# Kernel optimization log

Hardware: AMD Instinct MI355X
Metric: run time of the kernel (lower is better)

## Reference

```python
import jax, jax.numpy as jnp
import numpy as np

B, L, D, H, F = 2, 1024, 1024, 16, 4096
DH = D // H
EPS = 1e-6


def _layernorm(x, g, b, eps=1e-5):
    m = jnp.mean(x, axis=-1, keepdims=True)
    v = jnp.mean((x - m) ** 2, axis=-1, keepdims=True)
    return (x - m) / jnp.sqrt(v + eps) * g + b


def setup_inputs() -> dict:
    key = jax.random.key(0)
    ks = jax.random.split(key, 12)

    def w(k, shape):
        return jax.random.normal(k, shape, dtype=jnp.float32) * 0.02

    return {
        "inputs": jax.random.normal(ks[0], (B, L, D), dtype=jnp.float32),
        "attn_mask": jnp.zeros((L, L), dtype=jnp.bool_),
        "Wq": w(ks[1], (D, D)), "bq": jnp.zeros((D,), jnp.float32),
        "Wk": w(ks[2], (D, D)), "bk": jnp.zeros((D,), jnp.float32),
        "Wv": w(ks[3], (D, D)), "bv": jnp.zeros((D,), jnp.float32),
        "Wo": w(ks[4], (D, D)), "bo": jnp.zeros((D,), jnp.float32),
        "ln1_g": jnp.ones((D,), jnp.float32), "ln1_b": jnp.zeros((D,), jnp.float32),
        "W1": w(ks[5], (D, F)), "b1": jnp.zeros((F,), jnp.float32),
        "W2": w(ks[6], (F, D)), "b2": jnp.zeros((D,), jnp.float32),
        "ln2_g": jnp.ones((D,), jnp.float32), "ln2_b": jnp.zeros((D,), jnp.float32),
    }


def _decoder_layer(inputs, Wq, bq, Wk, bk, Wv, bv, Wo, bo,
                   ln1_g, ln1_b, W1, b1, W2, b2, ln2_g, ln2_b):
    Bn, Ln, Dn = inputs.shape

    def heads(W, b):
        # [B,L,D] -> [B,H,L,Dh]
        return (inputs @ W + b).reshape(Bn, Ln, H, DH).transpose(0, 2, 1, 3)

    q = jax.nn.sigmoid(heads(Wq, bq))  # kernel feature map
    k = jax.nn.sigmoid(heads(Wk, bk))
    v = heads(Wv, bv)

    normal = (jnp.arange(Ln, dtype=jnp.float32) + 1.0)[None, None, :]  # [1,1,L]

    sink_in = normal / jnp.einsum('bhld,bhld->bhl', q + EPS, jnp.cumsum(k, axis=2) + EPS)
    src_out = normal / jnp.einsum('bhld,bhld->bhl', k + EPS, jnp.cumsum(q, axis=2) + EPS)

    cons_sink = jnp.einsum('bhld,bhld->bhl', q + EPS,
                           jnp.cumsum(k * src_out[..., None], axis=2) + EPS) / normal
    cons_src = jnp.einsum('bhld,bhld->bhl', k + EPS,
                          jnp.cumsum(q * sink_in[..., None], axis=2) + EPS) / normal
    cons_src = jnp.clip(cons_src, -1.0, 1.0)

    sink_alloc = jax.nn.sigmoid(cons_sink)
    cons_src = jnp.exp(cons_src)
    src_comp = cons_src / jnp.cumsum(cons_src, axis=-1) * normal

    # causal linear attention: cumsum of outer products k v^T, contracted with q
    qs = q * (sink_in / normal)[..., None]           # [B,H,L,Dh]
    vs = v * src_comp[..., None]                     # [B,H,L,Dh]
    kv = jnp.cumsum(jnp.einsum('bhld,bhlm->bhldm', k, vs), axis=2)  # [B,H,L,Dh,Dh]
    x = jnp.einsum('bhld,bhldm->bhlm', qs, kv) * sink_alloc[..., None]

    x = x.transpose(0, 2, 1, 3).reshape(Bn, Ln, Dn)
    attn = x @ Wo + bo

    h = _layernorm(inputs + attn, ln1_g, ln1_b)
    ffn = jax.nn.gelu(h @ W1 + b1, approximate=False) @ W2 + b2
    return _layernorm(h + ffn, ln2_g, ln2_b)


def reference(inputs, attn_mask, Wq, bq, Wk, bk, Wv, bv, Wo, bo,
              ln1_g, ln1_b, W1, b1, W2, b2, ln2_g, ln2_b):
    # attn_mask is unused by the original module (causality comes from cumsum)
    return _decoder_layer(inputs, Wq, bq, Wk, bk, Wv, bv, Wo, bo,
                          ln1_g, ln1_b, W1, b1, W2, b2, ln2_g, ln2_b)
```

## Files before the change

### kernel.cpp

```cpp
#include <hip/hip_runtime.h>
#include <hip/hip_bf16.h>

#define EPS 1e-6f
#define NBH 32
#define LSEQ 1024
#define DHD 64

typedef unsigned short u16;
typedef __bf16 bf16x8 __attribute__((ext_vector_type(8)));
typedef float f32x4 __attribute__((ext_vector_type(4)));

__device__ inline u16 f2bf(float f){
  union { float f; unsigned u; } un; un.f = f;
  unsigned u = un.u;
  u += 0x7fffu + ((u >> 16) & 1u);
  return (u16)(u >> 16);
}

__device__ inline float wred64(float v){
#pragma unroll
  for (int off = 32; off > 0; off >>= 1) v += __shfl_xor(v, off, 64);
  return v;
}

__device__ inline float wscan64(float v, int lane){
  float run = v;
#pragma unroll
  for (int off = 1; off < 64; off <<= 1){
    float t = __shfl_up(run, off, 64);
    if (lane >= off) run += t;
  }
  return run;
}

__device__ inline float fast_sigmoid(float x){
  return 1.f / (1.f + __expf(-x));
}

__device__ inline void gload_lds16(const u16* g, u16* l){
  __builtin_amdgcn_global_load_lds(
      (const __attribute__((address_space(1))) unsigned int*)g,
      (__attribute__((address_space(3))) unsigned int*)l, 16, 0, 0);
}

__global__ __launch_bounds__(256) void f2bf_kernel(const float* __restrict__ in,
                                                   u16* __restrict__ out, int n4){
  int i = blockIdx.x * 256 + threadIdx.x;
  if (i < n4){
    float4 v = reinterpret_cast<const float4*>(in)[i];
    ushort4 o; o.x = f2bf(v.x); o.y = f2bf(v.y); o.z = f2bf(v.z); o.w = f2bf(v.w);
    reinterpret_cast<ushort4*>(out)[i] = o;
  }
}

__device__ inline void tr_tile2(const float* in, u16* out, int R, int C, int r0, int c0){
  __shared__ float tile[32][33];
  int x = threadIdx.x & 31, y = threadIdx.x >> 5;
#pragma unroll
  for (int j = 0; j < 4; j++)
    tile[y + j*8][x] = in[(size_t)(r0 + y + j*8) * C + c0 + x];
  __syncthreads();
#pragma unroll
  for (int j = 0; j < 4; j++)
    out[(size_t)(c0 + y + j*8) * R + r0 + x] = f2bf(tile[x][y + j*8]);
}

__global__ __launch_bounds__(256) void transpose4_f2bf(
    const float* __restrict__ w0, const float* __restrict__ w1,
    const float* __restrict__ w2, const float* __restrict__ w3,
    u16* __restrict__ dqkv, u16* __restrict__ dwo){
  int z = blockIdx.z;
  const float* in = (z == 0) ? w0 : (z == 1) ? w1 : (z == 2) ? w2 : w3;
  u16* out = (z < 3) ? (dqkv + (size_t)z * 1024 * 1024) : dwo;
  tr_tile2(in, out, 1024, 1024, blockIdx.y * 32, blockIdx.x * 32);
}

__global__ __launch_bounds__(256) void transpose2_f2bf(
    const float* __restrict__ w1, const float* __restrict__ w2,
    u16* __restrict__ d1, u16* __restrict__ d2){
  if (blockIdx.z == 0)
    tr_tile2(w1, d1, 1024, 4096, blockIdx.y * 32, blockIdx.x * 32);
  else
    tr_tile2(w2, d2, 4096, 1024, blockIdx.x * 32, blockIdx.y * 32);
}

__global__ __launch_bounds__(256) void bias_gather(const float* __restrict__ bq,
                                                   const float* __restrict__ bk,
                                                   const float* __restrict__ bv,
                                                   float* __restrict__ dst){
  int i = blockIdx.x * 256 + threadIdx.x;
  if (i < 3072){
    float v = (i < 1024) ? bq[i] : (i < 2048) ? bk[i - 1024] : bv[i - 2048];
    dst[i] = v;
  }
}

template<int BM, int BN, int ACT, int OM>
__global__ __launch_bounds__(256) void gemm_mfma(
    const u16* __restrict__ A, const u16* __restrict__ Bt,
    const float* __restrict__ bias, const float* __restrict__ resid,
    float* __restrict__ outF, u16* __restrict__ outB,
    int M, int N, int K)
{
  constexpr int BK = 64;
  constexpr int MI = BM / 32;
  constexpr int NJ = BN / 32;
  constexpr int RA = BM / 32;
  constexpr int RB = BN / 32;
  __shared__ u16 As[BM * BK];
  __shared__ u16 Bs[BN * BK];
  const int tid = threadIdx.x;
  const int lane = tid & 63, wave = tid >> 6;
  const int lrow = lane & 15, lg = lane >> 4;
  const int m0 = blockIdx.x * BM, n0 = blockIdx.y * BN;
  const int wm = (wave >> 1) * (BM / 2), wn = (wave & 1) * (BN / 2);

  const int ksz = K / gridDim.z;
  const int k_begin = blockIdx.z * ksz;
  const int k_end = k_begin + ksz;

  f32x4 acc[MI][NJ];
#pragma unroll
  for (int i = 0; i < MI; i++)
#pragma unroll
    for (int j = 0; j < NJ; j++) acc[i][j] = (f32x4){0.f, 0.f, 0.f, 0.f};

  const u16* Ab = A + (size_t)m0 * K;
  const u16* Bb = Bt + (size_t)n0 * K;

  const int s0 = ((0 * 4 + lg) ^ (lrow & 7)) * 8;
  const int s1 = ((1 * 4 + lg) ^ (lrow & 7)) * 8;

  for (int k0 = k_begin; k0 < k_end; k0 += BK){
    __syncthreads();
#pragma unroll
    for (int r = 0; r < RA; ++r){
      int c = r * 256 + tid;
      int row = c >> 3;
      int kk = ((c ^ row) & 7) << 3;
      gload_lds16(Ab + (size_t)row * K + k0 + kk, &As[(r * 256 + wave * 64) * 8]);
    }
#pragma unroll
    for (int r = 0; r < RB; ++r){
      int c = r * 256 + tid;
      int row = c >> 3;
      int kk = ((c ^ row) & 7) << 3;
      gload_lds16(Bb + (size_t)row * K + k0 + kk, &Bs[(r * 256 + wave * 64) * 8]);
    }
    __syncthreads();
#pragma unroll
    for (int kh = 0; kh < 2; ++kh){
      const int ss = (kh == 0) ? s0 : s1;
      bf16x8 af[MI], bfv[NJ];
#pragma unroll
      for (int i = 0; i < MI; ++i)
        af[i] = *reinterpret_cast<const bf16x8*>(&As[(wm + i * 16 + lrow) * BK + ss]);
#pragma unroll
      for (int j = 0; j < NJ; ++j)
        bfv[j] = *reinterpret_cast<const bf16x8*>(&Bs[(wn + j * 16 + lrow) * BK + ss]);
#pragma unroll
      for (int i = 0; i < MI; ++i)
#pragma unroll
        for (int j = 0; j < NJ; ++j)
          acc[i][j] = __builtin_amdgcn_mfma_f32_16x16x32_bf16(af[i], bfv[j], acc[i][j], 0, 0, 0);
    }
  }

#pragma unroll
  for (int i = 0; i < MI; ++i){
#pragma unroll
    for (int j = 0; j < NJ; ++j){
      int col = n0 + wn + j * 16 + lrow;
      float bv = (OM != 4 && bias) ? bias[col] : 0.f;
#pragma unroll
      for (int r = 0; r < 4; ++r){
        int row = m0 + wm + i * 16 + lg * 4 + r;
        float x = acc[i][j][r] + bv;
        if (OM == 1){
          if (col < 2048) x = fast_sigmoid(x);
          int which = col >> 10, cc = col & 1023, h = cc >> 6, d = cc & 63;
          int b = row >> 10, l = row & 1023;
          outF[(size_t)which * (2048ull * 1024) +
               (((size_t)(b * 16 + h)) * 1024 + l) * 64 + d] = x;
        } else if (OM == 4){
          outF[((size_t)blockIdx.z * M + row) * N + col] = x;
        } else {
          if (ACT == 2){
            float u = 0.7978845608f * (x + 0.044715f * x * x * x);
            float e = __expf(2.f * u);
            x = 0.5f * x * (2.f - 2.f / (e + 1.f));
          }
          outB[(size_t)row * N + col] = f2bf(x);
        }
      }
    }
  }
}

__global__ __launch_bounds__(256) void chunk_sums(const float* __restrict__ k, const float* __restrict__ q,
                                                  float* __restrict__ ck, float* __restrict__ cq){
  int blk = blockIdx.x;
  int lane = threadIdx.x & 63, wave = threadIdx.x >> 6;
  size_t base = (size_t)blk * 64 * DHD;
  float sk = 0.f, sq = 0.f;
  for (int l = wave * 16; l < wave * 16 + 16; l++){
    sk += k[base + l * 64 + lane];
    sq += q[base + l * 64 + lane];
  }
  __shared__ float rd[2][4][64];
  rd[0][wave][lane] = sk; rd[1][wave][lane] = sq;
  __syncthreads();
  if (wave == 0){
    ck[(size_t)blk * 64 + lane] = rd[0][0][lane] + rd[0][1][lane] + rd[0][2][lane] + rd[0][3][lane];
    cq[(size_t)blk * 64 + lane] = rd[1][0][lane] + rd[1][1][lane] + rd[1][2][lane] + rd[1][3][lane];
  }
}

__global__ __launch_bounds__(256) void sink_tile(
    const float* __restrict__ q, const float* __restrict__ k,
    const float* __restrict__ ck, const float* __restrict__ cq,
    float* __restrict__ sink_in, float* __restrict__ src_out,
    float* __restrict__ cso, float* __restrict__ cqsi)
{
  int blk = blockIdx.x, bh = blk >> 4, c = blk & 15;
  int tid = threadIdx.x, lane = tid & 63, wave = tid >> 6;
  __shared__ float qT[64][65], kT[64][65], G[64][66];
  __shared__ float PK[64], PQ[64];
  __shared__ float rk[64], rq[64], crk[64], crq[64], siv[64], sov[64];
  __shared__ float rd[2][4][64];
  size_t base = ((size_t)bh * LSEQ + c * 64) * DHD;
  const float* qb = q + base; const float* kb = k + base;
  for (int c4 = tid; c4 < 1024; c4 += 256){
    int l = c4 >> 4, d0 = (c4 & 15) * 4;
    float4 qv = *reinterpret_cast<const float4*>(qb + c4 * 4);
    qT[d0+0][l] = qv.x; qT[d0+1][l] = qv.y; qT[d0+2][l] = qv.z; qT[d0+3][l] = qv.w;
    float4 kv = *reinterpret_cast<const float4*>(kb + c4 * 4);
    kT[d0+0][l] = kv.x; kT[d0+1][l] = kv.y; kT[d0+2][l] = kv.z; kT[d0+3][l] = kv.w;
  }
  if (tid < 64){
    float pk = 0.f, pq = 0.f;
    for (int cc = 0; cc < c; cc++){
      pk += ck[((size_t)bh * 16 + cc) * 64 + tid];
      pq += cq[((size_t)bh * 16 + cc) * 64 + tid];
    }
    PK[tid] = pk; PQ[tid] = pq;
  }
  __syncthreads();
  float sumPK = wred64(PK[lane]);
  float sumPQ = wred64(PQ[lane]);
  {
    int l = lane, g = wave;
    float qrow[64];
#pragma unroll
    for (int d = 0; d < 64; d++) qrow[d] = qT[d][l];
    float p[16] = {};
    for (int d = 0; d < 64; d++){
      float qv = qrow[d];
#pragma unroll
      for (int j4 = 0; j4 < 4; j4++){
        float4 kk = *reinterpret_cast<const float4*>(&kT[d][g * 16 + j4 * 4]);
        p[j4*4+0] += qv * kk.x; p[j4*4+1] += qv * kk.y;
        p[j4*4+2] += qv * kk.z; p[j4*4+3] += qv * kk.w;
      }
    }
#pragma unroll
    for (int jj = 0; jj < 16; jj++) G[l][g * 16 + jj] = p[jj];
  }
  {
    float pk_ = 0.f, pq_ = 0.f;
#pragma unroll
    for (int d = wave * 16; d < wave * 16 + 16; d++){
      pk_ += kT[d][lane]; pq_ += qT[d][lane];
    }
    rd[0][wave][lane] = pk_; rd[1][wave][lane] = pq_;
  }
  __syncthreads();
  if (tid < 64){
    rk[tid] = rd[0][0][tid] + rd[0][1][tid] + rd[0][2][tid] + rd[0][3][tid];
    rq[tid] = rd[1][0][tid] + rd[1][1][tid] + rd[1][2][tid] + rd[1][3][tid];
  }
  __syncthreads();
  if (wave == 0)      crk[lane] = wscan64(rk[lane], lane);
  else if (wave == 1) crq[lane] = wscan64(rq[lane], lane);
  __syncthreads();
  {
    int l = lane;
    float p1 = 0.f, p2 = 0.f;
#pragma unroll
    for (int j = wave * 16; j < wave * 16 + 16; j++){
      float g1 = (j <= l) ? G[l][j] : 0.f;
      p1 += g1 + qT[j][l] * PK[j];
      float g2 = (j <= l) ? G[j][l] : 0.f;
      p2 += g2 + kT[j][l] * PQ[j];
    }
    rd[0][wave][l] = p1; rd[1][wave][l] = p2;
  }
  __syncthreads();
  const float EPS2 = 64.f * EPS * EPS;
  if (tid < 64){
    int l = tid;
    float s1 = rd[0][0][l] + rd[0][1][l] + rd[0][2][l] + rd[0][3][l];
    float s2 = rd[1][0][l] + rd[1][1][l] + rd[1][2][l] + rd[1][3][l];
    int L = c * 64 + l; float nrm = (float)(L + 1);
    float den1 = s1 + EPS * rq[l] + EPS * (sumPK + crk[l]) + EPS2;
    float den2 = s2 + EPS * rk[l] + EPS * (sumPQ + crq[l]) + EPS2;
    float si_ = nrm / den1, so_ = nrm / den2;
    sink_in[(size_t)bh * LSEQ + L] = si_;
    src_out[(size_t)bh * LSEQ + L] = so_;
    siv[l] = si_; sov[l] = so_;
  }
  __syncthreads();
  float s1 = 0.f, s2 = 0.f;
  for (int l = wave * 16; l < wave * 16 + 16; l++){
    s1 += sov[l] * kT[lane][l];
    s2 += siv[l] * qT[lane][l];
  }
  rd[0][wave][lane] = s1; rd[1][wave][lane] = s2;
  __syncthreads();
  if (wave == 0){
    cso [(size_t)blk * 64 + lane] = rd[0][0][lane] + rd[0][1][lane] + rd[0][2][lane] + rd[0][3][lane];
    cqsi[(size_t)blk * 64 + lane] = rd[1][0][lane] + rd[1][1][lane] + rd[1][2][lane] + rd[1][3][lane];
  }
}

__global__ __launch_bounds__(256) void cons_tile(
    const float* __restrict__ q, const float* __restrict__ k,
    const float* __restrict__ cso, const float* __restrict__ cqsi,
    const float* __restrict__ sink_in, const float* __restrict__ src_out,
    float* __restrict__ sa, float* __restrict__ ebuf)
{
  int blk = blockIdx.x, bh = blk >> 4, c = blk & 15;
  int tid = threadIdx.x, lane = tid & 63, wave = tid >> 6;
  __shared__ float qT[64][65], kT[64][65], G[64][66];
  __shared__ float PKso[64], PQsi[64];
  __shared__ float rk[64], rq[64], cwrk[64], cwrq[64], siv[64], sov[64];
  __shared__ float rd[2][4][64];
  size_t base = ((size_t)bh * LSEQ + c * 64) * DHD;
  const float* qb = q + base; const float* kb = k + base;
  for (int c4 = tid; c4 < 1024; c4 += 256){
    int l = c4 >> 4, d0 = (c4 & 15) * 4;
    float4 qv = *reinterpret_cast<const float4*>(qb + c4 * 4);
    qT[d0+0][l] = qv.x; qT[d0+1][l] = qv.y; qT[d0+2][l] = qv.z; qT[d0+3][l] = qv.w;
    float4 kv = *reinterpret_cast<const float4*>(kb + c4 * 4);
    kT[d0+0][l] = kv.x; kT[d0+1][l] = kv.y; kT[d0+2][l] = kv.z; kT[d0+3][l] = kv.w;
  }
  if (tid < 64){
    float pk = 0.f, pq = 0.f;
    for (int cc = 0; cc < c; cc++){
      pk += cso [((size_t)bh * 16 + cc) * 64 + tid];
      pq += cqsi[((size_t)bh * 16 + cc) * 64 + tid];
    }
    PKso[tid] = pk; PQsi[tid] = pq;
  } else if (tid < 128){
    int l = tid - 64;
    sov[l] = src_out[(size_t)bh * LSEQ + c * 64 + l];
    siv[l] = sink_in[(size_t)bh * LSEQ + c * 64 + l];
  }
  __syncthreads();
  float sumPKso = wred64(PKso[lane]);
  float sumPQsi = wred64(PQsi[lane]);
  {
    int l = lane, g = wave;
    float qrow[64];
#pragma unroll
    for (int d = 0; d < 64; d++) qrow[d] = qT[d][l];
    float p[16] = {};
    for (int d = 0; d < 64; d++){
      float qv = qrow[d];
#pragma unroll
      for (int j4 = 0; j4 < 4; j4++){
        float4 kk = *reinterpret_cast<const float4*>(&kT[d][g * 16 + j4 * 4]);
        p[j4*4+0] += qv * kk.x; p[j4*4+1] += qv * kk.y;
        p[j4*4+2] += qv * kk.z; p[j4*4+3] += qv * kk.w;
      }
    }
#pragma unroll
    for (int jj = 0; jj < 16; jj++) G[l][g * 16 + jj] = p[jj];
  }
  {
    float pk_ = 0.f, pq_ = 0.f;
#pragma unroll
    for (int d = wave * 16; d < wave * 16 + 16; d++){
      pk_ += kT[d][lane]; pq_ += qT[d][lane];
    }
    rd[0][wave][lane] = pk_; rd[1][wave][lane] = pq_;
  }
  __syncthreads();
  if (tid < 64){
    rk[tid] = rd[0][0][tid] + rd[0][1][tid] + rd[0][2][tid] + rd[0][3][tid];
    rq[tid] = rd[1][0][tid] + rd[1][1][tid] + rd[1][2][tid] + rd[1][3][tid];
  }
  __syncthreads();
  if (wave == 0)      cwrk[lane] = wscan64(sov[lane] * rk[lane], lane);
  else if (wave == 1) cwrq[lane] = wscan64(siv[lane] * rq[lane], lane);
  __syncthreads();
  {
    int l = lane;
    float p3 = 0.f, p4 = 0.f;
#pragma unroll
    for (int j = wave * 16; j < wave * 16 + 16; j++){
      float g3 = (j <= l) ? sov[j] * G[l][j] : 0.f;
      p3 += g3 + qT[j][l] * PKso[j];
      float g4 = (j <= l) ? siv[j] * G[j][l] : 0.f;
      p4 += g4 + kT[j][l] * PQsi[j];
    }
    rd[0][wave][l] = p3; rd[1][wave][l] = p4;
  }
  __syncthreads();
  const float EPS2 = 64.f * EPS * EPS;
  if (tid < 64){
    int l = tid;
    float s3 = rd[0][0][l] + rd[0][1][l] + rd[0][2][l] + rd[0][3][l];
    float s4 = rd[1][0][l] + rd[1][1][l] + rd[1][2][l] + rd[1][3][l];
    int L = c * 64 + l; float nrm = (float)(L + 1);
    float cs = (s3 + EPS * rq[l] + EPS * (sumPKso + cwrk[l]) + EPS2) / nrm;
    sa[(size_t)bh * LSEQ + L] = fast_sigmoid(cs);
    float c2 = (s4 + EPS * rk[l] + EPS * (sumPQsi + cwrq[l]) + EPS2) / nrm;
    c2 = fminf(1.f, fmaxf(-1.f, c2));
    ebuf[(size_t)bh * LSEQ + L] = __expf(c2);
  }
}

__global__ __launch_bounds__(64) void srccomp_kernel(const float* __restrict__ ebuf, float* __restrict__ sc){
  int bh = blockIdx.x; int lane = threadIdx.x;
  const float* eb = ebuf + (size_t)bh * LSEQ;
  float loc[16]; float s = 0.f;
#pragma unroll
  for (int i = 0; i < 16; i++){ loc[i] = eb[lane * 16 + i]; s += loc[i]; }
  float run = wscan64(s, lane);
  float acc = run - s;
  float* scb = sc + (size_t)bh * LSEQ;
#pragma unroll
  for (int i = 0; i < 16; i++){
    acc += loc[i];
    scb[lane * 16 + i] = loc[i] / acc * (float)(lane * 16 + i + 1);
  }
}

__global__ __launch_bounds__(256) void phaseA(const float* __restrict__ k, const float* __restrict__ v,
                                              const float* __restrict__ sc, float* __restrict__ S){
  int blk = blockIdx.x; int bh = blk >> 4, c = blk & 15;
  __shared__ float ks[64][68], vss[64][68];
  __shared__ float vc[64];
  int tid = threadIdx.x;
  size_t base = ((size_t)bh * LSEQ + c * 64) * DHD;
  const float* kb = k + base; const float* vb = v + base;
  if (tid < 64) vc[tid] = sc[(size_t)bh * LSEQ + c * 64 + tid];
  __syncthreads();
  for (int c4 = tid; c4 < 1024; c4 += 256){
    int l = c4 >> 4, d0 = (c4 & 15) * 4;
    *reinterpret_cast<float4*>(&ks[l][d0]) = *reinterpret_cast<const float4*>(kb + c4 * 4);
    float4 vv = *reinterpret_cast<const float4*>(vb + c4 * 4);
    float w = vc[l];
    vss[l][d0+0] = vv.x * w; vss[l][d0+1] = vv.y * w;
    vss[l][d0+2] = vv.z * w; vss[l][d0+3] = vv.w * w;
  }
  __syncthreads();
  int m = tid >> 2, dg = tid & 3;
  float acc[16] = {};
  for (int l = 0; l < 64; l++){
    float vm = vss[l][m];
#pragma unroll
    for (int d4 = 0; d4 < 4; d4++){
      float4 kk = *reinterpret_cast<const float4*>(&ks[l][dg * 16 + d4 * 4]);
      acc[d4*4+0] += vm * kk.x; acc[d4*4+1] += vm * kk.y;
      acc[d4*4+2] += vm * kk.z; acc[d4*4+3] += vm * kk.w;
    }
  }
  float* Sb = S + (size_t)blk * 4096 + m * 64 + dg * 16;
#pragma unroll
  for (int d4 = 0; d4 < 4; d4++)
    *reinterpret_cast<float4*>(Sb + d4 * 4) =
        make_float4(acc[d4*4], acc[d4*4+1], acc[d4*4+2], acc[d4*4+3]);
}

__global__ __launch_bounds__(256) void phaseB(const float* __restrict__ S, float* __restrict__ KVp){
  int blk = blockIdx.x; int bh = blk >> 4, c = blk & 15;
  int off = threadIdx.x * 16;
  float acc[16] = {};
  for (int cc = 0; cc < c; cc++){
    size_t idx = ((size_t)bh * 16 + cc) * 4096 + off;
#pragma unroll
    for (int t = 0; t < 4; t++){
      float4 sv = *reinterpret_cast<const float4*>(S + idx + t * 4);
      acc[t*4] += sv.x; acc[t*4+1] += sv.y; acc[t*4+2] += sv.z; acc[t*4+3] += sv.w;
    }
  }
  size_t oidx = ((size_t)bh * 16 + c) * 4096 + off;
#pragma unroll
  for (int t = 0; t < 4; t++)
    *reinterpret_cast<float4*>(KVp + oidx + t * 4) =
        make_float4(acc[t*4], acc[t*4+1], acc[t*4+2], acc[t*4+3]);
}

__global__ __launch_bounds__(256) void phaseC(const float* __restrict__ q, const float* __restrict__ k,
                                              const float* __restrict__ v, const float* __restrict__ KVp,
                                              const float* __restrict__ sink_in, const float* __restrict__ sc,
                                              const float* __restrict__ sa, u16* __restrict__ x){
  int blk = blockIdx.x; int bh = blk >> 4, c = blk & 15;
  int b = bh >> 4, h = bh & 15;
  __shared__ float qsT[64][65];
  __shared__ float kT[64][68];
  __shared__ float vss[64][68];
  __shared__ float kvs[64][68];
  __shared__ float Ps[64][66];
  __shared__ float qc[64], vc[64];
  int tid = threadIdx.x;
  size_t base = ((size_t)bh * LSEQ + c * 64) * DHD;
  const float* qb = q + base; const float* kb = k + base; const float* vb = v + base;
  const float* kvb = KVp + (size_t)blk * 4096;
  if (tid < 64){
    int L = c * 64 + tid;
    qc[tid] = sink_in[(size_t)bh * LSEQ + L] / (float)(L + 1);
    vc[tid] = sc[(size_t)bh * LSEQ + L];
  }
  __syncthreads();
  for (int c4 = tid; c4 < 1024; c4 += 256){
    int l = c4 >> 4, d0 = (c4 & 15) * 4;
    float qw = qc[l], vw = vc[l];
    float4 qv = *reinterpret_cast<const float4*>(qb + c4 * 4);
    qsT[d0+0][l] = qv.x * qw; qsT[d0+1][l] = qv.y * qw;
    qsT[d0+2][l] = qv.z * qw; qsT[d0+3][l] = qv.w * qw;
    float4 kv4 = *reinterpret_cast<const float4*>(kb + c4 * 4);
    kT[d0+0][l] = kv4.x; kT[d0+1][l] = kv4.y; kT[d0+2][l] = kv4.z; kT[d0+3][l] = kv4.w;
    float4 vv = *reinterpret_cast<const float4*>(vb + c4 * 4);
    vss[l][d0+0] = vv.x * vw; vss[l][d0+1] = vv.y * vw;
    vss[l][d0+2] = vv.z * vw; vss[l][d0+3] = vv.w * vw;
    *reinterpret_cast<float4*>(&kvs[l][d0]) = *reinterpret_cast<const float4*>(kvb + c4 * 4);
  }
  __syncthreads();
  int l = tid & 63, g = tid >> 6;
  float qrow[64];
#pragma unroll
  for (int d = 0; d < 64; d++) qrow[d] = qsT[d][l];

  float p[16] = {};
  for (int d = 0; d < 64; d++){
    float qv = qrow[d];
#pragma unroll
    for (int j4 = 0; j4 < 4; j4++){
      float4 kk = *reinterpret_cast<const float4*>(&kT[d][g * 16 + j4 * 4]);
      p[j4*4+0] += qv * kk.x; p[j4*4+1] += qv * kk.y;
      p[j4*4+2] += qv * kk.z; p[j4*4+3] += qv * kk.w;
    }
  }
#pragma unroll
  for (int jj = 0; jj < 16; jj++){
    int j = g * 16 + jj;
    Ps[l][j] = (j <= l) ? p[jj] : 0.f;
  }
  __syncthreads();

  float acc[16];
#pragma unroll
  for (int mm = 0; mm < 16; mm++){
    float a = 0.f;
#pragma unroll
    for (int d4 = 0; d4 < 16; d4++){
      float4 kv4 = *reinterpret_cast<const float4*>(&kvs[g * 16 + mm][d4 * 4]);
      a += qrow[d4*4+0]*kv4.x + qrow[d4*4+1]*kv4.y + qrow[d4*4+2]*kv4.z + qrow[d4*4+3]*kv4.w;
    }
    acc[mm] = a;
  }
  for (int j = 0; j < 64; j++){
    float pv = Ps[l][j];
#pragma unroll
    for (int m4 = 0; m4 < 4; m4++){
      float4 vv = *reinterpret_cast<const float4*>(&vss[j][g * 16 + m4 * 4]);
      acc[m4*4+0] += pv * vv.x; acc[m4*4+1] += pv * vv.y;
      acc[m4*4+2] += pv * vv.z; acc[m4*4+3] += pv * vv.w;
    }
  }
  float sav = sa[(size_t)bh * LSEQ + c * 64 + l];
  u16* xo = x + ((size_t)(b * 1024 + c * 64 + l)) * 1024 + h * 64 + g * 16;
#pragma unroll
  for (int mm = 0; mm < 16; mm++) xo[mm] = f2bf(acc[mm] * sav);
}

__global__ __launch_bounds__(256) void ln_fused2b(
    const float* __restrict__ p0, const float* __restrict__ p1,
    const float* __restrict__ resid, const float* __restrict__ bias,
    const float* __restrict__ g, const float* __restrict__ b,
    float* __restrict__ out, u16* __restrict__ outbf){
  int row = blockIdx.x; int tid = threadIdx.x;
  int lane = tid & 63, wave = tid >> 6;
  size_t off = (size_t)row * 1024 + tid * 4;
  float4 a0 = *reinterpret_cast<const float4*>(p0 + off);
  float4 a1 = *reinterpret_cast<const float4*>(p1 + off);
  float4 rr = *reinterpret_cast<const float4*>(resid + off);
  float4 bb = *reinterpret_cast<const float4*>(bias + tid * 4);
  float4 v = make_float4(a0.x + a1.x + rr.x + bb.x, a0.y + a1.y + rr.y + bb.y,
                         a0.z + a1.z + rr.z + bb.z, a0.w + a1.w + rr.w + bb.w);
  float s = v.x + v.y + v.z + v.w;
  float s2 = v.x*v.x + v.y*v.y + v.z*v.z + v.w*v.w;
  s = wred64(s); s2 = wred64(s2);
  __shared__ float red[2][4];
  if (lane == 0){ red[0][wave] = s; red[1][wave] = s2; }
  __syncthreads();
  float S = red[0][0] + red[0][1] + red[0][2] + red[0][3];
  float S2 = red[1][0] + red[1][1] + red[1][2] + red[1][3];
  float mean = S * (1.f / 1024.f);
  float var = S2 * (1.f / 1024.f) - mean * mean;
  float inv = rsqrtf(var + 1e-5f);
  float4 gv = *reinterpret_cast<const float4*>(g + tid * 4);
  float4 bv = *reinterpret_cast<const float4*>(b + tid * 4);
  float y0 = (v.x - mean) * inv * gv.x + bv.x;
  float y1 = (v.y - mean) * inv * gv.y + bv.y;
  float y2 = (v.z - mean) * inv * gv.z + bv.z;
  float y3 = (v.w - mean) * inv * gv.w + bv.w;
  *reinterpret_cast<float4*>(out + off) = make_float4(y0, y1, y2, y3);
  ushort4 o; o.x = f2bf(y0); o.y = f2bf(y1); o.z = f2bf(y2); o.w = f2bf(y3);
  *reinterpret_cast<ushort4*>(outbf + off) = o;
}

__global__ __launch_bounds__(256) void ln_fused4(
    const float* __restrict__ p0, const float* __restrict__ p1,
    const float* __restrict__ p2, const float* __restrict__ p3,
    const float* __restrict__ resid, const float* __restrict__ bias,
    const float* __restrict__ g, const float* __restrict__ b,
    float* __restrict__ out){
  int row = blockIdx.x; int tid = threadIdx.x;
  int lane = tid & 63, wave = tid >> 6;
  size_t off = (size_t)row * 1024 + tid * 4;
  float4 a0 = *reinterpret_cast<const float4*>(p0 + off);
  float4 a1 = *reinterpret_cast<const float4*>(p1 + off);
  float4 a2 = *reinterpret_cast<const float4*>(p2 + off);
  float4 a3 = *reinterpret_cast<const float4*>(p3 + off);
  float4 rr = *reinterpret_cast<const float4*>(resid + off);
  float4 bb = *reinterpret_cast<const float4*>(bias + tid * 4);
  float4 v = make_float4(a0.x + a1.x + a2.x + a3.x + rr.x + bb.x,
                         a0.y + a1.y + a2.y + a3.y + rr.y + bb.y,
                         a0.z + a1.z + a2.z + a3.z + rr.z + bb.z,
                         a0.w + a1.w + a2.w + a3.w + rr.w + bb.w);
  float s = v.x + v.y + v.z + v.w;
  float s2 = v.x*v.x + v.y*v.y + v.z*v.z + v.w*v.w;
  s = wred64(s); s2 = wred64(s2);
  __shared__ float red[2][4];
  if (lane == 0){ red[0][wave] = s; red[1][wave] = s2; }
  __syncthreads();
  float S = red[0][0] + red[0][1] + red[0][2] + red[0][3];
  float S2 = red[1][0] + red[1][1] + red[1][2] + red[1][3];
  float mean = S * (1.f / 1024.f);
  float var = S2 * (1.f / 1024.f) - mean * mean;
  float inv = rsqrtf(var + 1e-5f);
  float4 gv = *reinterpret_cast<const float4*>(g + tid * 4);
  float4 bv = *reinterpret_cast<const float4*>(b + tid * 4);
  float y0 = (v.x - mean) * inv * gv.x + bv.x;
  float y1 = (v.y - mean) * inv * gv.y + bv.y;
  float y2 = (v.z - mean) * inv * gv.z + bv.z;
  float y3 = (v.w - mean) * inv * gv.w + bv.w;
  *reinterpret_cast<float4*>(out + off) = make_float4(y0, y1, y2, y3);
}

extern "C" void kernel_launch(void* const* d_in, const int* in_sizes, int n_in,
                              void* d_out, int out_size, void* d_ws, size_t ws_size,
                              hipStream_t stream){
  (void)in_sizes; (void)n_in; (void)out_size; (void)ws_size;
  const float* inputs = (const float*)d_in[0];
  const float* Wq = (const float*)d_in[2];  const float* bq = (const float*)d_in[3];
  const float* Wk = (const float*)d_in[4];  const float* bk = (const float*)d_in[5];
  const float* Wv = (const float*)d_in[6];  const float* bv = (const float*)d_in[7];
  const float* Wo = (const float*)d_in[8];  const float* bo = (const float*)d_in[9];
  const float* ln1g = (const float*)d_in[10]; const float* ln1b = (const float*)d_in[11];
  const float* W1 = (const float*)d_in[12]; const float* b1 = (const float*)d_in[13];
  const float* W2 = (const float*)d_in[14]; const float* b2 = (const float*)d_in[15];
  const float* ln2g = (const float*)d_in[16]; const float* ln2b = (const float*)d_in[17];
  float* out = (float*)d_out;

  char* wsp = (char*)d_ws; size_t off = 0;
  auto alloc = [&](size_t bytes) -> void* {
    off = (off + 255) & ~(size_t)255;
    void* p = wsp + off; off += bytes; return p;
  };
  const size_t MD = (size_t)2048 * 1024;
  u16* Xbf    = (u16*)alloc(MD * 2);
  u16* WqkvT  = (u16*)alloc((size_t)3 * 1024 * 1024 * 2);
  u16* WoT    = (u16*)alloc((size_t)1024 * 1024 * 2);
  u16* W1T    = (u16*)alloc((size_t)4096 * 1024 * 2);
  u16* W2T    = (u16*)alloc((size_t)4096 * 1024 * 2);
  float* bqkv = (float*)alloc(3072 * 4);
  float* qkvb = (float*)alloc(3 * MD * 4);
  float* qb = qkvb; float* kb = qkvb + MD; float* vb = qkvb + 2 * MD;
  float* quad = (float*)alloc(4 * MD * 4);
  float* Sbuf = quad;
  float* KVp  = quad + MD;
  float* ckb  = (float*)alloc((size_t)512 * 64 * 4);
  float* cqb  = (float*)alloc((size_t)512 * 64 * 4);
  float* csob = (float*)alloc((size_t)512 * 64 * 4);
  float* cqsib= (float*)alloc((size_t)512 * 64 * 4);
  float* sink_in = (float*)alloc(NBH * LSEQ * 4);
  float* src_out = (float*)alloc(NBH * LSEQ * 4);
  float* sabuf   = (float*)alloc(NBH * LSEQ * 4);
  float* ebuf    = (float*)alloc(NBH * LSEQ * 4);
  float* scbuf   = (float*)alloc(NBH * LSEQ * 4);
  u16* xatt   = (u16*)alloc(MD * 2);
  u16* g1     = (u16*)alloc((size_t)2048 * 4096 * 2);
  float* part = quad;
  float* hbuf = vb;
  u16* hbf = (u16*)qb;

  f2bf_kernel<<<2048, 256, 0, stream>>>(inputs, Xbf, (int)(MD / 4));
  transpose4_f2bf<<<dim3(32, 32, 4), 256, 0, stream>>>(Wq, Wk, Wv, Wo, WqkvT, WoT);
  transpose2_f2bf<<<dim3(128, 32, 2), 256, 0, stream>>>(W1, W2, W1T, W2T);
  bias_gather<<<12, 256, 0, stream>>>(bq, bk, bv, bqkv);

  gemm_mfma<128, 64, 0, 1><<<dim3(16, 48), 256, 0, stream>>>(
      Xbf, WqkvT, bqkv, nullptr, qkvb, nullptr, 2048, 3072, 1024);

  chunk_sums<<<512, 256, 0, stream>>>(kb, qb, ckb, cqb);
  sink_tile<<<512, 256, 0, stream>>>(qb, kb, ckb, cqb, sink_in, src_out, csob, cqsib);
  cons_tile<<<512, 256, 0, stream>>>(qb, kb, csob, cqsib, sink_in, src_out, sabuf, ebuf);
  srccomp_kernel<<<32, 64, 0, stream>>>(ebuf, scbuf);

  phaseA<<<512, 256, 0, stream>>>(kb, vb, scbuf, Sbuf);
  phaseB<<<512, 256, 0, stream>>>(Sbuf, KVp);
  phaseC<<<512, 256, 0, stream>>>(qb, kb, vb, KVp, sink_in, scbuf, sabuf, xatt);

  gemm_mfma<128, 64, 0, 4><<<dim3(16, 16, 2), 256, 0, stream>>>(
      xatt, WoT, nullptr, nullptr, part, nullptr, 2048, 1024, 1024);
  ln_fused2b<<<2048, 256, 0, stream>>>(part, part + MD, inputs, bo, ln1g, ln1b, hbuf, hbf);

  gemm_mfma<128, 128, 2, 3><<<dim3(16, 32), 256, 0, stream>>>(
      hbf, W1T, b1, nullptr, nullptr, g1, 2048, 4096, 1024);
  gemm_mfma<128, 128, 0, 4><<<dim3(16, 8, 4), 256, 0, stream>>>(
      g1, W2T, nullptr, nullptr, part, nullptr, 2048, 1024, 4096);
  ln_fused4<<<2048, 256, 0, stream>>>(part, part + MD, part + 2 * MD, part + 3 * MD,
                                      hbuf, b2, ln2g, ln2b, out);
}
```

Before: 221.6 us.

## Double-buffer LDS tiles in MFMA GEMM to overlap global loads with compute

Converts the GEMM main loop from single-buffered to double-buffered shared memory. The next K tile is prefetched with direct global-to-LDS loads while the current tile is consumed. Partial vmcnt waits let only the older stage's loads complete before the barrier. The aim is to hide global memory latency behind the MFMA work. In exchange it doubles LDS use per block, which may lower occupancy, and it depends on the hand-written vmcnt counts matching the number of issued loads.

```diff
diff --git a/kernel.cpp b/kernel.cpp
--- a/kernel.cpp
+++ b/kernel.cpp
@@ -107,8 +107,9 @@
   constexpr int NJ = BN / 32;
   constexpr int RA = BM / 32;
   constexpr int RB = BN / 32;
-  __shared__ u16 As[BM * BK];
-  __shared__ u16 Bs[BN * BK];
+  constexpr int NS = RA + RB;
+  __shared__ u16 As[2][BM * BK];
+  __shared__ u16 Bs[2][BN * BK];
   const int tid = threadIdx.x;
   const int lane = tid & 63, wave = tid >> 6;
   const int lrow = lane & 15, lg = lane >> 4;
@@ -131,39 +132,54 @@
   const int s0 = ((0 * 4 + lg) ^ (lrow & 7)) * 8;
   const int s1 = ((1 * 4 + lg) ^ (lrow & 7)) * 8;
 
-  for (int k0 = k_begin; k0 < k_end; k0 += BK){
-    __syncthreads();
+  auto STAGE = [&](int buf, int k0){
 #pragma unroll
     for (int r = 0; r < RA; ++r){
       int c = r * 256 + tid;
       int row = c >> 3;
       int kk = ((c ^ row) & 7) << 3;
-      gload_lds16(Ab + (size_t)row * K + k0 + kk, &As[(r * 256 + wave * 64) * 8]);
+      gload_lds16(Ab + (size_t)row * K + k0 + kk, &As[buf][(r * 256 + wave * 64) * 8]);
     }
 #pragma unroll
     for (int r = 0; r < RB; ++r){
       int c = r * 256 + tid;
       int row = c >> 3;
       int kk = ((c ^ row) & 7) << 3;
-      gload_lds16(Bb + (size_t)row * K + k0 + kk, &Bs[(r * 256 + wave * 64) * 8]);
-    }
-    __syncthreads();
+      gload_lds16(Bb + (size_t)row * K + k0 + kk, &Bs[buf][(r * 256 + wave * 64) * 8]);
+    }
+  };
+
+  STAGE(0, k_begin);
+  int cur = 0;
+  for (int k0 = k_begin; k0 < k_end; k0 += BK){
+    if (k0 + BK < k_end){
+      STAGE(cur ^ 1, k0 + BK);
+      if constexpr (NS == 8)      asm volatile("s_waitcnt vmcnt(8)" ::: "memory");
+      else if constexpr (NS == 6) asm volatile("s_waitcnt vmcnt(6)" ::: "memory");
+      else                        asm volatile("s_waitcnt vmcnt(0)" ::: "memory");
+    } else {
+      asm volatile("s_waitcnt vmcnt(0)" ::: "memory");
+    }
+    __builtin_amdgcn_s_barrier();
+    __builtin_amdgcn_sched_barrier(0);
 #pragma unroll
     for (int kh = 0; kh < 2; ++kh){
       const int ss = (kh == 0) ? s0 : s1;
       bf16x8 af[MI], bfv[NJ];
 #pragma unroll
       for (int i = 0; i < MI; ++i)
-        af[i] = *reinterpret_cast<const bf16x8*>(&As[(wm + i * 16 + lrow) * BK + ss]);
+        af[i] = *reinterpret_cast<const bf16x8*>(&As[cur][(wm + i * 16 + lrow) * BK + ss]);
 #pragma unroll
       for (int j = 0; j < NJ; ++j)
-        bfv[j] = *reinterpret_cast<const bf16x8*>(&Bs[(wn + j * 16 + lrow) * BK + ss]);
+        bfv[j] = *reinterpret_cast<const bf16x8*>(&Bs[cur][(wn + j * 16 + lrow) * BK + ss]);
 #pragma unroll
       for (int i = 0; i < MI; ++i)
 #pragma unroll
         for (int j = 0; j < NJ; ++j)
           acc[i][j] = __builtin_amdgcn_mfma_f32_16x16x32_bf16(af[i], bfv[j], acc[i][j], 0, 0, 0);
     }
+    __builtin_amdgcn_s_barrier();
+    cur ^= 1;
   }
 
 #pragma unroll
```

Result: faster. 216.3 us (-2.4%).
